# Kernel tuning notes

Measured on AMD Instinct MI355X. Metric: run time of the kernel, lower is better.

The kernel has to match this reference:

```python
import jax, jax.numpy as jnp
import numpy as np

NUM_HEADS = 16


def setup_inputs() -> dict:
    key = jax.random.key(0)
    ks = jax.random.split(key, 5)
    B, S, H = 2, 2048, 1024
    scale = 0.02
    return {
        "x": jax.random.normal(ks[0], (B, S, H), dtype=jnp.float32),
        "w_qkv": jax.random.normal(ks[1], (H, 3 * H), dtype=jnp.float32) * scale,
        "b_qkv": jax.random.normal(ks[2], (3 * H,), dtype=jnp.float32) * scale,
        "w_out": jax.random.normal(ks[3], (H, H), dtype=jnp.float32) * scale,
        "b_out": jax.random.normal(ks[4], (H,), dtype=jnp.float32) * scale,
    }


def reference(x, w_qkv, b_qkv, w_out, b_out):
    B, S, H = x.shape
    nh = NUM_HEADS
    hd = H // nh
    attn_scale = 1.0 / np.sqrt(hd).astype(np.float32)

    qkv = x @ w_qkv + b_qkv                       # (B, S, 3H)
    q, k, v = jnp.split(qkv, 3, axis=-1)
    # (B, S, H) -> (B, nh, S, hd)
    to_heads = lambda t: t.reshape(B, S, nh, hd).transpose(0, 2, 1, 3)
    q, k, v = to_heads(q), to_heads(k), to_heads(v)

    scores = jnp.einsum("bhid,bhjd->bhij", q, k) * attn_scale  # (B, nh, S, S)
    # Source masks where triu(ones)==0 -> strictly-lower triangle masked;
    # allowed positions are j >= i (attends to present and future).
    i = jnp.arange(S)[:, None]
    j = jnp.arange(S)[None, :]
    scores = jnp.where(j >= i, scores, -jnp.inf)
    attn = jax.nn.softmax(scores, axis=-1)        # dropout is identity (eval)

    out = jnp.einsum("bhij,bhjd->bhid", attn, v)  # (B, nh, S, hd)
    out = out.transpose(0, 2, 1, 3).reshape(B, S, H)
    return out @ w_out + b_out
```

## Files before the change

kernel.cpp:

```cpp
#include <hip/hip_runtime.h>
#include <hip/hip_bf16.h>
#include <stdint.h>
#include <stddef.h>

typedef __bf16 bf16_t;
typedef __bf16 bf16x4 __attribute__((ext_vector_type(4)));
typedef __bf16 bf16x8 __attribute__((ext_vector_type(8)));
typedef float f32x4 __attribute__((ext_vector_type(4)));

#define MFMA16(a, b, c) __builtin_amdgcn_mfma_f32_16x16x32_bf16(a, b, c, 0, 0, 0)

#define GLL16(g, l)                                                      \
    __builtin_amdgcn_global_load_lds(                                    \
        (const __attribute__((address_space(1))) void*)(g),              \
        (__attribute__((address_space(3))) void*)(l), 16, 0, 0)

#define SEQ 2048
#define NHEAD 16
#define HD 64
#define HID 1024
#define QKV_LD 3072
#define VT_LD 2080

__global__ __launch_bounds__(256)
void prep_kernel(const float* __restrict__ x, const float* __restrict__ w_qkv,
                 const float* __restrict__ w_out, bf16_t* __restrict__ xbf,
                 bf16_t* __restrict__ wqkvT, bf16_t* __restrict__ woutT) {
    int L = blockIdx.x;
    int tid = threadIdx.x;
    if (L < 4096) {
        int i = (L * 256 + tid) * 4;
        float4 v = *(const float4*)(x + i);
        bf16x4 o = {(bf16_t)v.x, (bf16_t)v.y, (bf16_t)v.z, (bf16_t)v.w};
        *(bf16x4*)(xbf + i) = o;
        return;
    }
    __shared__ bf16_t tile[32][33];
    const float* W;
    bf16_t* Wt;
    int N, bx, by;
    if (L < 7168) {
        int r = L - 4096;
        W = w_qkv; Wt = wqkvT; N = 3072; bx = r % 96; by = r / 96;
    } else {
        int r = L - 7168;
        W = w_out; Wt = woutT; N = 1024; bx = r % 32; by = r / 32;
    }
    int K = 1024;
    int n0 = bx * 32, k0 = by * 32;
    int tx = tid & 31, ty = tid >> 5;
#pragma unroll
    for (int i = 0; i < 4; i++)
        tile[ty + i * 8][tx] = (bf16_t)W[(size_t)(k0 + ty + i * 8) * N + n0 + tx];
    __syncthreads();
#pragma unroll
    for (int i = 0; i < 4; i++)
        Wt[(size_t)(n0 + ty + i * 8) * K + k0 + tx] = tile[tx][ty + i * 8];
}

__global__ __launch_bounds__(256)
void vt_transpose(const bf16_t* __restrict__ qkv, bf16_t* __restrict__ Vt) {
    int s0 = blockIdx.x * 64;
    int bh = blockIdx.y;
    int b = bh >> 4, h = bh & 15;
    int tid = threadIdx.x;
    __shared__ __align__(16) bf16_t tile[64][72];

    int row = tid >> 3, c8 = (tid & 7) * 8;
#pragma unroll
    for (int it = 0; it < 2; it++) {
        int sr = row + it * 32;
        bf16x8 v = *(const bf16x8*)(qkv + ((size_t)b * SEQ + s0 + sr) * QKV_LD +
                                    2 * HID + h * HD + c8);
        *(bf16x8*)(&tile[sr][c8]) = v;
    }
    __syncthreads();
#pragma unroll
    for (int it = 0; it < 2; it++) {
        int d = row + it * 32;
        bf16x8 w;
#pragma unroll
        for (int e = 0; e < 8; e++) w[e] = tile[c8 + e][d];
        *(bf16x8*)(Vt + ((size_t)bh * HD + d) * VT_LD + s0 + c8) = w;
    }
}

template <typename OutT, int TN>
__global__ __launch_bounds__(256)
void gemm_bt_bias(const bf16_t* __restrict__ A, const bf16_t* __restrict__ Bt,
                  const float* __restrict__ bias, OutT* __restrict__ C,
                  int M, int N, int K) {
    constexpr int NT = TN / 32;
    __shared__ __align__(16) bf16_t As[128][32];
    __shared__ __align__(16) bf16_t Bs[TN][32];

    int m0 = blockIdx.y * 128;
    int n0 = blockIdx.x * TN;
    int tid = threadIdx.x;
    int wave = tid >> 6, lane = tid & 63;
    int quad = lane >> 4, l16 = lane & 15;
    int wm = (wave >> 1) * 64, wn = (wave & 1) * (TN / 2);

    f32x4 acc[4][NT] = {};

    const bf16_t* a_base =
        A + (size_t)(m0 + wave * 32 + (lane >> 2)) * K + (lane & 3) * 8;
    const bf16_t* b_base =
        Bt + (size_t)(n0 + wave * (TN / 4) + (lane >> 2)) * K + (lane & 3) * 8;
    bf16_t* as_base = &As[wave * 32][0];
    bf16_t* bs_base = &Bs[wave * (TN / 4)][0];

    for (int k0 = 0; k0 < K; k0 += 32) {
        GLL16(a_base + k0, as_base);
        GLL16(a_base + 16 * K + k0, as_base + 16 * 32);
        GLL16(b_base + k0, bs_base);
        if (TN == 128) GLL16(b_base + 16 * K + k0, bs_base + 16 * 32);
        __syncthreads();

        bf16x8 af[4], bfr[NT];
#pragma unroll
        for (int t = 0; t < 4; t++)
            af[t] = *(const bf16x8*)(&As[wm + t * 16 + l16][quad * 8]);
#pragma unroll
        for (int t = 0; t < NT; t++)
            bfr[t] = *(const bf16x8*)(&Bs[wn + t * 16 + l16][quad * 8]);
#pragma unroll
        for (int mt = 0; mt < 4; mt++)
#pragma unroll
            for (int nt = 0; nt < NT; nt++)
                acc[mt][nt] = MFMA16(af[mt], bfr[nt], acc[mt][nt]);
        __syncthreads();
    }

#pragma unroll
    for (int mt = 0; mt < 4; mt++) {
        int row = m0 + wm + mt * 16 + quad * 4;
#pragma unroll
        for (int nt = 0; nt < NT; nt++) {
            int col = n0 + wn + nt * 16 + l16;
            float bv = bias[col];
#pragma unroll
            for (int r = 0; r < 4; r++)
                C[(size_t)(row + r) * N + col] = (OutT)(acc[mt][nt][r] + bv);
        }
    }
}

__global__ __launch_bounds__(256)
void attn_kernel(const bf16_t* __restrict__ qkv, const bf16_t* __restrict__ Vt,
                 bf16_t* __restrict__ attn_out) {
    int bh = blockIdx.x;
    int tile = blockIdx.y;
    int b = bh >> 4, h = bh & 15;

    int tid = threadIdx.x, wave = tid >> 6, lane = tid & 63;
    int quad = lane >> 4, l16 = lane & 15;

    const bf16_t* q_g = qkv + (size_t)b * SEQ * QKV_LD + (size_t)h * HD;
    const bf16_t* k_g = q_g + HID;
    const bf16_t* vt_g = Vt + (size_t)bh * HD * VT_LD;

    __shared__ __align__(16) bf16_t Ks[128][72];
    __shared__ __align__(16) bf16_t Vs[64][136];
    __shared__ __align__(16) bf16_t Ps[4][16][136];

    bf16x8 ones;
#pragma unroll
    for (int e = 0; e < 8; e++) ones[e] = (bf16_t)1.0f;

    int krow = tid >> 3, kc8 = (tid & 7) * 8;
    int vrow = tid >> 4, vc8 = (tid & 15) * 8;
    const float QS = 0.125f * 1.44269504088896f;

    int i0 = tile * 64;
    int iw = i0 + wave * 16;

    bf16x8 qa0, qa1;
    {
        bf16x8 t0 = *(const bf16x8*)(q_g + (size_t)(iw + l16) * QKV_LD + quad * 8);
        bf16x8 t1 = *(const bf16x8*)(q_g + (size_t)(iw + l16) * QKV_LD + 32 + quad * 8);
#pragma unroll
        for (int e = 0; e < 8; e++) {
            qa0[e] = (bf16_t)((float)t0[e] * QS);
            qa1[e] = (bf16_t)((float)t1[e] * QS);
        }
    }

    f32x4 o[4] = {};
    f32x4 lacc = {};

    int jstart = i0 & ~127;

    bf16x8 kr[4], vr[4];
#pragma unroll
    for (int t = 0; t < 4; t++) {
        kr[t] = *(const bf16x8*)(k_g + (size_t)(jstart + krow + t * 32) * QKV_LD + kc8);
        vr[t] = *(const bf16x8*)(vt_g + (size_t)(vrow + t * 16) * VT_LD + jstart + vc8);
    }

    for (int j0 = jstart; j0 < SEQ; j0 += 128) {
        __syncthreads();
#pragma unroll
        for (int t = 0; t < 4; t++) {
            *(bf16x8*)(&Ks[krow + t * 32][kc8]) = kr[t];
            *(bf16x8*)(&Vs[vrow + t * 16][vc8]) = vr[t];
        }
        __syncthreads();

        if (j0 + 128 < SEQ) {
#pragma unroll
            for (int t = 0; t < 4; t++) {
                kr[t] = *(const bf16x8*)(k_g + (size_t)(j0 + 128 + krow + t * 32) * QKV_LD + kc8);
                vr[t] = *(const bf16x8*)(vt_g + (size_t)(vrow + t * 16) * VT_LD + j0 + 128 + vc8);
            }
        }

        f32x4 s[8];
#pragma unroll
        for (int jt = 0; jt < 8; jt++) {
            bf16x8 kb0 = *(const bf16x8*)(&Ks[jt * 16 + l16][quad * 8]);
            bf16x8 kb1 = *(const bf16x8*)(&Ks[jt * 16 + l16][32 + quad * 8]);
            f32x4 a = {};
            a = MFMA16(qa0, kb0, a);
            a = MFMA16(qa1, kb1, a);
            s[jt] = a;
        }

        if (j0 == jstart) {
#pragma unroll
            for (int jt = 0; jt < 8; jt++) {
                int gj = j0 + jt * 16 + l16;
#pragma unroll
                for (int r = 0; r < 4; r++) {
                    int gi = iw + quad * 4 + r;
                    float p = (gj >= gi) ? __builtin_amdgcn_exp2f(s[jt][r]) : 0.0f;
                    Ps[wave][quad * 4 + r][jt * 16 + l16] = (bf16_t)p;
                }
            }
        } else {
#pragma unroll
            for (int jt = 0; jt < 8; jt++)
#pragma unroll
                for (int r = 0; r < 4; r++)
                    Ps[wave][quad * 4 + r][jt * 16 + l16] =
                        (bf16_t)__builtin_amdgcn_exp2f(s[jt][r]);
        }

        bf16x8 pa[4];
#pragma unroll
        for (int kk = 0; kk < 4; kk++) {
            pa[kk] = *(const bf16x8*)(&Ps[wave][l16][kk * 32 + quad * 8]);
            lacc = MFMA16(pa[kk], ones, lacc);
        }

#pragma unroll
        for (int nt = 0; nt < 4; nt++) {
#pragma unroll
            for (int kk = 0; kk < 4; kk++) {
                bf16x8 vb = *(const bf16x8*)(&Vs[nt * 16 + l16][kk * 32 + quad * 8]);
                o[nt] = MFMA16(pa[kk], vb, o[nt]);
            }
        }
    }

#pragma unroll
    for (int r = 0; r < 4; r++) {
        int gi = iw + quad * 4 + r;
        float inv = 1.0f / lacc[r];
#pragma unroll
        for (int nt = 0; nt < 4; nt++)
            attn_out[(size_t)(b * SEQ + gi) * HID + h * HD + nt * 16 + l16] =
                (bf16_t)(o[nt][r] * inv);
    }
}

extern "C" void kernel_launch(void* const* d_in, const int* in_sizes, int n_in,
                              void* d_out, int out_size, void* d_ws, size_t ws_size,
                              hipStream_t stream) {
    const float* x     = (const float*)d_in[0];
    const float* w_qkv = (const float*)d_in[1];
    const float* b_qkv = (const float*)d_in[2];
    const float* w_out = (const float*)d_in[3];
    const float* b_out = (const float*)d_in[4];
    float* out = (float*)d_out;

    char* ws = (char*)d_ws;
    bf16_t* xbf   = (bf16_t*)(ws);
    bf16_t* Vt    = (bf16_t*)(ws);
    bf16_t* wqkvT = (bf16_t*)(ws + 8388608);
    bf16_t* woutT = (bf16_t*)(ws + 14680064);
    bf16_t* qkv   = (bf16_t*)(ws + 16777216);
    bf16_t* attn  = (bf16_t*)(ws + 41943040);

    prep_kernel<<<8192, 256, 0, stream>>>(x, w_qkv, w_out, xbf, wqkvT, woutT);

    gemm_bt_bias<bf16_t, 128><<<dim3(3072 / 128, 4096 / 128), 256, 0, stream>>>(
        xbf, wqkvT, b_qkv, qkv, 4096, 3072, 1024);

    vt_transpose<<<dim3(SEQ / 64, 2 * NHEAD), 256, 0, stream>>>(qkv, Vt);

    attn_kernel<<<dim3(2 * NHEAD, SEQ / 64), 256, 0, stream>>>(qkv, Vt, attn);

    gemm_bt_bias<float, 64><<<dim3(1024 / 64, 4096 / 128), 256, 0, stream>>>(
        attn, woutT, b_out, out, 4096, 1024, 1024);
}
```

Measured before the change: 187.9 us.

## Process 32 query rows per wave with register row sums and heavy-first tile order

```diff
diff --git a/kernel.cpp b/kernel.cpp
--- a/kernel.cpp
+++ b/kernel.cpp
@@ -149,8 +149,10 @@
 __global__ __launch_bounds__(256)
 void attn_kernel(const bf16_t* __restrict__ qkv, const bf16_t* __restrict__ Vt,
                  bf16_t* __restrict__ attn_out) {
-    int bh = blockIdx.x;
-    int tile = blockIdx.y;
+    int L = blockIdx.x;
+    int half = L >> 8, r5 = L & 255;
+    int bh = r5 & 31;
+    int tile = half ? (15 - (r5 >> 5)) : (r5 >> 5);
     int b = bh >> 4, h = bh & 15;
 
     int tid = threadIdx.x, wave = tid >> 6, lane = tid & 63;
@@ -162,34 +164,32 @@
 
     __shared__ __align__(16) bf16_t Ks[128][72];
     __shared__ __align__(16) bf16_t Vs[64][136];
-    __shared__ __align__(16) bf16_t Ps[4][16][136];
-
-    bf16x8 ones;
-#pragma unroll
-    for (int e = 0; e < 8; e++) ones[e] = (bf16_t)1.0f;
+    __shared__ __align__(16) bf16_t Ps[4][32][136];
 
     int krow = tid >> 3, kc8 = (tid & 7) * 8;
     int vrow = tid >> 4, vc8 = (tid & 15) * 8;
     const float QS = 0.125f * 1.44269504088896f;
 
-    int i0 = tile * 64;
-    int iw = i0 + wave * 16;
-
-    bf16x8 qa0, qa1;
-    {
-        bf16x8 t0 = *(const bf16x8*)(q_g + (size_t)(iw + l16) * QKV_LD + quad * 8);
-        bf16x8 t1 = *(const bf16x8*)(q_g + (size_t)(iw + l16) * QKV_LD + 32 + quad * 8);
+    int i0 = tile * 128;
+    int iwb = i0 + wave * 32;
+
+    bf16x8 qa[2][2];
+#pragma unroll
+    for (int g = 0; g < 2; g++) {
+        const bf16_t* qrow = q_g + (size_t)(iwb + g * 16 + l16) * QKV_LD;
+        bf16x8 t0 = *(const bf16x8*)(qrow + quad * 8);
+        bf16x8 t1 = *(const bf16x8*)(qrow + 32 + quad * 8);
 #pragma unroll
         for (int e = 0; e < 8; e++) {
-            qa0[e] = (bf16_t)((float)t0[e] * QS);
-            qa1[e] = (bf16_t)((float)t1[e] * QS);
-        }
-    }
-
-    f32x4 o[4] = {};
-    f32x4 lacc = {};
-
-    int jstart = i0 & ~127;
+            qa[g][0][e] = (bf16_t)((float)t0[e] * QS);
+            qa[g][1][e] = (bf16_t)((float)t1[e] * QS);
+        }
+    }
+
+    f32x4 o[2][4] = {};
+    float lsum[2] = {0.0f, 0.0f};
+
+    int jstart = i0;
 
     bf16x8 kr[4], vr[4];
 #pragma unroll
@@ -215,62 +215,90 @@
             }
         }
 
-        f32x4 s[8];
+        f32x4 s[2][8];
 #pragma unroll
         for (int jt = 0; jt < 8; jt++) {
             bf16x8 kb0 = *(const bf16x8*)(&Ks[jt * 16 + l16][quad * 8]);
             bf16x8 kb1 = *(const bf16x8*)(&Ks[jt * 16 + l16][32 + quad * 8]);
-            f32x4 a = {};
-            a = MFMA16(qa0, kb0, a);
-            a = MFMA16(qa1, kb1, a);
-            s[jt] = a;
+#pragma unroll
+            for (int g = 0; g < 2; g++) {
+                f32x4 a = {};
+                a = MFMA16(kb0, qa[g][0], a);
+                a = MFMA16(kb1, qa[g][1], a);
+                s[g][jt] = a;
+            }
         }
 
         if (j0 == jstart) {
 #pragma unroll
-            for (int jt = 0; jt < 8; jt++) {
-                int gj = j0 + jt * 16 + l16;
-#pragma unroll
-                for (int r = 0; r < 4; r++) {
-                    int gi = iw + quad * 4 + r;
-                    float p = (gj >= gi) ? __builtin_amdgcn_exp2f(s[jt][r]) : 0.0f;
-                    Ps[wave][quad * 4 + r][jt * 16 + l16] = (bf16_t)p;
+            for (int g = 0; g < 2; g++) {
+                int gi = iwb + g * 16 + l16;
+#pragma unroll
+                for (int jt = 0; jt < 8; jt++) {
+                    bf16x4 pk;
+#pragma unroll
+                    for (int r = 0; r < 4; r++) {
+                        int gj = j0 + jt * 16 + quad * 4 + r;
+                        float p = (gj >= gi) ? __builtin_amdgcn_exp2f(s[g][jt][r]) : 0.0f;
+                        lsum[g] += p;
+                        pk[r] = (bf16_t)p;
+                    }
+                    *(bf16x4*)(&Ps[wave][g * 16 + l16][jt * 16 + quad * 4]) = pk;
                 }
             }
         } else {
 #pragma unroll
-            for (int jt = 0; jt < 8; jt++)
-#pragma unroll
-                for (int r = 0; r < 4; r++)
-                    Ps[wave][quad * 4 + r][jt * 16 + l16] =
-                        (bf16_t)__builtin_amdgcn_exp2f(s[jt][r]);
-        }
-
-        bf16x8 pa[4];
-#pragma unroll
-        for (int kk = 0; kk < 4; kk++) {
-            pa[kk] = *(const bf16x8*)(&Ps[wave][l16][kk * 32 + quad * 8]);
-            lacc = MFMA16(pa[kk], ones, lacc);
-        }
+            for (int g = 0; g < 2; g++) {
+#pragma unroll
+                for (int jt = 0; jt < 8; jt++) {
+                    bf16x4 pk;
+#pragma unroll
+                    for (int r = 0; r < 4; r++) {
+                        float p = __builtin_amdgcn_exp2f(s[g][jt][r]);
+                        lsum[g] += p;
+                        pk[r] = (bf16_t)p;
+                    }
+                    *(bf16x4*)(&Ps[wave][g * 16 + l16][jt * 16 + quad * 4]) = pk;
+                }
+            }
+        }
+
+        bf16x8 pa[2][4];
+#pragma unroll
+        for (int g = 0; g < 2; g++)
+#pragma unroll
+            for (int kk = 0; kk < 4; kk++)
+                pa[g][kk] = *(const bf16x8*)(&Ps[wave][g * 16 + l16][kk * 32 + quad * 8]);
 
 #pragma unroll
         for (int nt = 0; nt < 4; nt++) {
 #pragma unroll
             for (int kk = 0; kk < 4; kk++) {
                 bf16x8 vb = *(const bf16x8*)(&Vs[nt * 16 + l16][kk * 32 + quad * 8]);
-                o[nt] = MFMA16(pa[kk], vb, o[nt]);
-            }
-        }
-    }
-
-#pragma unroll
-    for (int r = 0; r < 4; r++) {
-        int gi = iw + quad * 4 + r;
-        float inv = 1.0f / lacc[r];
-#pragma unroll
-        for (int nt = 0; nt < 4; nt++)
-            attn_out[(size_t)(b * SEQ + gi) * HID + h * HD + nt * 16 + l16] =
-                (bf16_t)(o[nt][r] * inv);
+#pragma unroll
+                for (int g = 0; g < 2; g++)
+                    o[g][nt] = MFMA16(pa[g][kk], vb, o[g][nt]);
+            }
+        }
+    }
+
+#pragma unroll
+    for (int g = 0; g < 2; g++) {
+        lsum[g] += __shfl_xor(lsum[g], 16, 64);
+        lsum[g] += __shfl_xor(lsum[g], 32, 64);
+    }
+#pragma unroll
+    for (int g = 0; g < 2; g++) {
+#pragma unroll
+        for (int r = 0; r < 4; r++) {
+            float rs = __shfl(lsum[g], quad * 4 + r, 64);
+            float inv = 1.0f / rs;
+            int gi = iwb + g * 16 + quad * 4 + r;
+#pragma unroll
+            for (int nt = 0; nt < 4; nt++)
+                attn_out[(size_t)(b * SEQ + gi) * HID + h * HD + nt * 16 + l16] =
+                    (bf16_t)(o[g][nt][r] * inv);
+        }
     }
 }
 
@@ -299,7 +327,7 @@
 
     vt_transpose<<<dim3(SEQ / 64, 2 * NHEAD), 256, 0, stream>>>(qkv, Vt);
 
-    attn_kernel<<<dim3(2 * NHEAD, SEQ / 64), 256, 0, stream>>>(qkv, Vt, attn);
+    attn_kernel<<<512, 256, 0, stream>>>(qkv, Vt, attn);
 
     gemm_bt_bias<float, 64><<<dim3(1024 / 64, 4096 / 128), 256, 0, stream>>>(
         attn, woutT, b_out, out, 4096, 1024, 1024);
```

Result: slower. 194.4 us (+3.5%).

## Restructure attention to 32x32 MFMA with 2x2 wave split and 64-key tiles

Applied to the files above, without the earlier changes.

```diff
diff --git a/kernel.cpp b/kernel.cpp
--- a/kernel.cpp
+++ b/kernel.cpp
@@ -7,8 +7,10 @@
 typedef __bf16 bf16x4 __attribute__((ext_vector_type(4)));
 typedef __bf16 bf16x8 __attribute__((ext_vector_type(8)));
 typedef float f32x4 __attribute__((ext_vector_type(4)));
+typedef float f32x16 __attribute__((ext_vector_type(16)));
 
 #define MFMA16(a, b, c) __builtin_amdgcn_mfma_f32_16x16x32_bf16(a, b, c, 0, 0, 0)
+#define MFMA32(a, b, c) __builtin_amdgcn_mfma_f32_32x32x16_bf16(a, b, c, 0, 0, 0)
 
 #define GLL16(g, l)                                                      \
     __builtin_amdgcn_global_load_lds(                                    \
@@ -154,123 +156,119 @@
     int b = bh >> 4, h = bh & 15;
 
     int tid = threadIdx.x, wave = tid >> 6, lane = tid & 63;
-    int quad = lane >> 4, l16 = lane & 15;
+    int l32 = lane & 31, hi = lane >> 5;
+    int ih = wave & 1, jh = wave >> 1;
 
     const bf16_t* q_g = qkv + (size_t)b * SEQ * QKV_LD + (size_t)h * HD;
     const bf16_t* k_g = q_g + HID;
     const bf16_t* vt_g = Vt + (size_t)bh * HD * VT_LD;
 
-    __shared__ __align__(16) bf16_t Ks[128][72];
-    __shared__ __align__(16) bf16_t Vs[64][136];
-    __shared__ __align__(16) bf16_t Ps[4][16][136];
-
-    bf16x8 ones;
-#pragma unroll
-    for (int e = 0; e < 8; e++) ones[e] = (bf16_t)1.0f;
-
-    int krow = tid >> 3, kc8 = (tid & 7) * 8;
-    int vrow = tid >> 4, vc8 = (tid & 15) * 8;
+    __shared__ __align__(16) bf16_t Ks[64][72];
+    __shared__ __align__(16) bf16_t Vs[64][72];
+    __shared__ __align__(16) bf16_t Ps[64][68];
+    __shared__ float lsumS[4][32];
+
     const float QS = 0.125f * 1.44269504088896f;
-
     int i0 = tile * 64;
-    int iw = i0 + wave * 16;
-
-    bf16x8 qa0, qa1;
+
+    bf16x8 qa[4];
     {
-        bf16x8 t0 = *(const bf16x8*)(q_g + (size_t)(iw + l16) * QKV_LD + quad * 8);
-        bf16x8 t1 = *(const bf16x8*)(q_g + (size_t)(iw + l16) * QKV_LD + 32 + quad * 8);
-#pragma unroll
-        for (int e = 0; e < 8; e++) {
-            qa0[e] = (bf16_t)((float)t0[e] * QS);
-            qa1[e] = (bf16_t)((float)t1[e] * QS);
-        }
-    }
-
-    f32x4 o[4] = {};
-    f32x4 lacc = {};
-
-    int jstart = i0 & ~127;
-
-    bf16x8 kr[4], vr[4];
-#pragma unroll
-    for (int t = 0; t < 4; t++) {
-        kr[t] = *(const bf16x8*)(k_g + (size_t)(jstart + krow + t * 32) * QKV_LD + kc8);
-        vr[t] = *(const bf16x8*)(vt_g + (size_t)(vrow + t * 16) * VT_LD + jstart + vc8);
-    }
-
-    for (int j0 = jstart; j0 < SEQ; j0 += 128) {
-        __syncthreads();
-#pragma unroll
-        for (int t = 0; t < 4; t++) {
-            *(bf16x8*)(&Ks[krow + t * 32][kc8]) = kr[t];
-            *(bf16x8*)(&Vs[vrow + t * 16][vc8]) = vr[t];
-        }
-        __syncthreads();
-
-        if (j0 + 128 < SEQ) {
-#pragma unroll
-            for (int t = 0; t < 4; t++) {
-                kr[t] = *(const bf16x8*)(k_g + (size_t)(j0 + 128 + krow + t * 32) * QKV_LD + kc8);
-                vr[t] = *(const bf16x8*)(vt_g + (size_t)(vrow + t * 16) * VT_LD + j0 + 128 + vc8);
+        const bf16_t* qrow = q_g + (size_t)(i0 + ih * 32 + l32) * QKV_LD + hi * 8;
+#pragma unroll
+        for (int ks = 0; ks < 4; ks++) {
+            bf16x8 t = *(const bf16x8*)(qrow + ks * 16);
+#pragma unroll
+            for (int e = 0; e < 8; e++) qa[ks][e] = (bf16_t)((float)t[e] * QS);
+        }
+    }
+
+    f32x16 o = {};
+    float lsum = 0.0f;
+
+    int sr = tid >> 2, sc = (tid & 3) * 8;
+
+    bf16x8 kr[2], vr[2];
+#pragma unroll
+    for (int t = 0; t < 2; t++) {
+        kr[t] = *(const bf16x8*)(k_g + (size_t)(i0 + sr) * QKV_LD + sc + t * 32);
+        vr[t] = *(const bf16x8*)(vt_g + (size_t)sr * VT_LD + i0 + sc + t * 32);
+    }
+
+    for (int j0 = i0; j0 < SEQ; j0 += 64) {
+        __syncthreads();
+#pragma unroll
+        for (int t = 0; t < 2; t++) {
+            *(bf16x8*)(&Ks[sr][sc + t * 32]) = kr[t];
+            *(bf16x8*)(&Vs[sr][sc + t * 32]) = vr[t];
+        }
+        __syncthreads();
+
+        if (j0 + 64 < SEQ) {
+#pragma unroll
+            for (int t = 0; t < 2; t++) {
+                kr[t] = *(const bf16x8*)(k_g + (size_t)(j0 + 64 + sr) * QKV_LD + sc + t * 32);
+                vr[t] = *(const bf16x8*)(vt_g + (size_t)sr * VT_LD + j0 + 64 + sc + t * 32);
             }
         }
 
-        f32x4 s[8];
-#pragma unroll
-        for (int jt = 0; jt < 8; jt++) {
-            bf16x8 kb0 = *(const bf16x8*)(&Ks[jt * 16 + l16][quad * 8]);
-            bf16x8 kb1 = *(const bf16x8*)(&Ks[jt * 16 + l16][32 + quad * 8]);
-            f32x4 a = {};
-            a = MFMA16(qa0, kb0, a);
-            a = MFMA16(qa1, kb1, a);
-            s[jt] = a;
-        }
-
-        if (j0 == jstart) {
-#pragma unroll
-            for (int jt = 0; jt < 8; jt++) {
-                int gj = j0 + jt * 16 + l16;
+        f32x16 st = {};
+#pragma unroll
+        for (int ks = 0; ks < 4; ks++) {
+            bf16x8 ka = *(const bf16x8*)(&Ks[jh * 32 + l32][ks * 16 + hi * 8]);
+            st = MFMA32(ka, qa[ks], st);
+        }
+
+        if (j0 == i0) {
+            int gi = i0 + ih * 32 + l32;
+#pragma unroll
+            for (int rq = 0; rq < 4; rq++) {
+                bf16x4 pk;
 #pragma unroll
                 for (int r = 0; r < 4; r++) {
-                    int gi = iw + quad * 4 + r;
-                    float p = (gj >= gi) ? __builtin_amdgcn_exp2f(s[jt][r]) : 0.0f;
-                    Ps[wave][quad * 4 + r][jt * 16 + l16] = (bf16_t)p;
+                    int gj = j0 + jh * 32 + 8 * rq + 4 * hi + r;
+                    float p = (gj >= gi) ? __builtin_amdgcn_exp2f(st[rq * 4 + r]) : 0.0f;
+                    lsum += p;
+                    pk[r] = (bf16_t)p;
                 }
+                *(bf16x4*)(&Ps[ih * 32 + l32][jh * 32 + 8 * rq + 4 * hi]) = pk;
             }
         } else {
 #pragma unroll
-            for (int jt = 0; jt < 8; jt++)
-#pragma unroll
-                for (int r = 0; r < 4; r++)
-                    Ps[wave][quad * 4 + r][jt * 16 + l16] =
-                        (bf16_t)__builtin_amdgcn_exp2f(s[jt][r]);
-        }
-
-        bf16x8 pa[4];
-#pragma unroll
-        for (int kk = 0; kk < 4; kk++) {
-            pa[kk] = *(const bf16x8*)(&Ps[wave][l16][kk * 32 + quad * 8]);
-            lacc = MFMA16(pa[kk], ones, lacc);
-        }
-
-#pragma unroll
-        for (int nt = 0; nt < 4; nt++) {
-#pragma unroll
-            for (int kk = 0; kk < 4; kk++) {
-                bf16x8 vb = *(const bf16x8*)(&Vs[nt * 16 + l16][kk * 32 + quad * 8]);
-                o[nt] = MFMA16(pa[kk], vb, o[nt]);
+            for (int rq = 0; rq < 4; rq++) {
+                bf16x4 pk;
+#pragma unroll
+                for (int r = 0; r < 4; r++) {
+                    float p = __builtin_amdgcn_exp2f(st[rq * 4 + r]);
+                    lsum += p;
+                    pk[r] = (bf16_t)p;
+                }
+                *(bf16x4*)(&Ps[ih * 32 + l32][jh * 32 + 8 * rq + 4 * hi]) = pk;
             }
         }
-    }
-
-#pragma unroll
-    for (int r = 0; r < 4; r++) {
-        int gi = iw + quad * 4 + r;
-        float inv = 1.0f / lacc[r];
-#pragma unroll
-        for (int nt = 0; nt < 4; nt++)
-            attn_out[(size_t)(b * SEQ + gi) * HID + h * HD + nt * 16 + l16] =
-                (bf16_t)(o[nt][r] * inv);
+        __syncthreads();
+
+#pragma unroll
+        for (int ks = 0; ks < 4; ks++) {
+            bf16x8 pa = *(const bf16x8*)(&Ps[ih * 32 + l32][ks * 16 + hi * 8]);
+            bf16x8 vb = *(const bf16x8*)(&Vs[jh * 32 + l32][ks * 16 + hi * 8]);
+            o = MFMA32(pa, vb, o);
+        }
+    }
+
+    lsum += __shfl_xor(lsum, 32, 64);
+    lsumS[wave][l32] = lsum;
+    __syncthreads();
+
+#pragma unroll
+    for (int rq = 0; rq < 4; rq++) {
+#pragma unroll
+        for (int r = 0; r < 4; r++) {
+            int il = 8 * rq + 4 * hi + r;
+            float rs = lsumS[ih][il] + lsumS[ih + 2][il];
+            int gi = i0 + ih * 32 + il;
+            attn_out[(size_t)(b * SEQ + gi) * HID + h * HD + jh * 32 + l32] =
+                (bf16_t)(o[rq * 4 + r] / rs);
+        }
     }
 }
 
```

Result: faster. 182.1 us (-3.1%).
